# Performance work log

Measured on AMD Instinct MI355X. Metric: run time of the kernel, lower is better.

## Reference

```python
import jax, jax.numpy as jnp
import numpy as np

B, S, D = 2, 2048, 1024
H = 16
DK = D // H  # attn_dim // num_heads = 64
DV = D // H  # embed_dim // num_heads = 64
NEG = -1e9


def setup_inputs() -> dict:
    key = jax.random.key(0)
    ks = jax.random.split(key, 6)
    inputs = jax.random.normal(ks[0], (B, S, D), dtype=jnp.float32)
    # mask[b, i, j]: key position i may attend to query position j when i <= j (causal)
    mask = jnp.broadcast_to(jnp.triu(jnp.ones((S, S), dtype=bool))[None], (B, S, S))
    sd = 1.0 / np.sqrt(D)
    WQ = jax.random.normal(ks[1], (D, H, DK), dtype=jnp.float32) * sd
    WK = jax.random.normal(ks[2], (D, H, DK), dtype=jnp.float32) * sd
    WV = jax.random.normal(ks[3], (D, H, DV), dtype=jnp.float32) * sd
    WO = jax.random.normal(ks[4], (D, D), dtype=jnp.float32) * sd
    bO = jnp.zeros((D,), dtype=jnp.float32)
    return {"inputs": inputs, "mask": mask, "WQ": WQ, "WK": WK, "WV": WV, "WO": WO, "bO": bO}


def reference(inputs, mask, WQ, WK, WV, WO, bO):
    scale = 1.0 / jnp.sqrt(jnp.float32(DK))
    q = jnp.einsum('bid,dhk->bihk', inputs, WQ) * scale
    k = jnp.einsum('bid,dhk->bihk', inputs, WK)
    v = jnp.einsum('bid,dhv->bihv', inputs, WV)
    # scores: [b, i, j, h]; softmax over axis=1 (key axis i), as in the original
    scores = jnp.einsum('bihd,bjhd->bijh', q, k)
    scores = jnp.where(mask[..., None], scores, NEG)
    attn = jax.nn.softmax(scores, axis=1)
    x = jnp.einsum('bijh,bihv->bjhv', attn, v)  # output indexed by query j
    x = x.reshape(B, S, D)
    return x @ WO + bO
```

## Files before the change

### kernel.cpp

```cpp
#include <hip/hip_runtime.h>
#include <hip/hip_bf16.h>


typedef __bf16 bf16;
typedef __bf16 bf16x8 __attribute__((ext_vector_type(8)));
typedef __bf16 bf16x4 __attribute__((ext_vector_type(4)));
typedef float  f32x4  __attribute__((ext_vector_type(4)));

constexpr int Sq = 2048;
constexpr int Dm = 1024;
constexpr int Hh = 16;

__global__ __launch_bounds__(256) void cvt_bf16(
    const float* __restrict__ src, bf16* __restrict__ dst, int n) {
  const int i = (blockIdx.x * 256 + threadIdx.x) * 8;
  if (i >= n) return;
  float4 a = *reinterpret_cast<const float4*>(src + i);
  float4 b = *reinterpret_cast<const float4*>(src + i + 4);
  bf16x8 o;
  o[0] = (bf16)a.x; o[1] = (bf16)a.y; o[2] = (bf16)a.z; o[3] = (bf16)a.w;
  o[4] = (bf16)b.x; o[5] = (bf16)b.y; o[6] = (bf16)b.z; o[7] = (bf16)b.w;
  *reinterpret_cast<bf16x8*>(dst + i) = o;
}

__global__ __launch_bounds__(256) void tposeW4(
    const float* __restrict__ WQ, const float* __restrict__ WK,
    const float* __restrict__ WV, const float* __restrict__ WO,
    bf16* __restrict__ out) {
  __shared__ bf16 t[64][65];
  const int z = blockIdx.z;
  const float* in = (z == 0) ? WQ : (z == 1) ? WK : (z == 2) ? WV : WO;
  bf16* op = out + (size_t)z * 1024 * 1024;
  const int r0 = blockIdx.y * 64, c0 = blockIdx.x * 64;
  const int tid = threadIdx.x;
  const int rr = tid >> 3, cc = (tid & 7) * 8;
#pragma unroll
  for (int it = 0; it < 2; ++it) {
    int row = rr + it * 32;
    const float* ip = in + (size_t)(r0 + row) * 1024 + c0 + cc;
    float4 a = *reinterpret_cast<const float4*>(ip);
    float4 b = *reinterpret_cast<const float4*>(ip + 4);
    t[row][cc + 0] = (bf16)a.x; t[row][cc + 1] = (bf16)a.y;
    t[row][cc + 2] = (bf16)a.z; t[row][cc + 3] = (bf16)a.w;
    t[row][cc + 4] = (bf16)b.x; t[row][cc + 5] = (bf16)b.y;
    t[row][cc + 6] = (bf16)b.z; t[row][cc + 7] = (bf16)b.w;
  }
  __syncthreads();
#pragma unroll
  for (int it = 0; it < 2; ++it) {
    int crow = rr + it * 32;
    alignas(16) bf16 o[8];
#pragma unroll
    for (int e = 0; e < 8; ++e) o[e] = t[cc + e][crow];
    *reinterpret_cast<bf16x8*>(op + (size_t)(c0 + crow) * 1024 + r0 + cc) =
        *reinterpret_cast<bf16x8*>(o);
  }
}

template <int EPI>
__global__ __launch_bounds__(256) void gemm128(
    const bf16* __restrict__ A, const bf16* __restrict__ Bt,
    const int M, const int N, const int K,
    bf16* __restrict__ Katt, bf16* __restrict__ Qatt, bf16* __restrict__ VattT,
    const float* __restrict__ bOf, float* __restrict__ Cout) {
  __shared__ bf16 As[8192], Bs[8192];
  const int tid = threadIdx.x;
  const int lane = tid & 63;
  const int w = tid >> 6;
  const int wr = w >> 1, wc = w & 1;
  const int g = lane >> 4, c = lane & 15;
  const int m0 = blockIdx.y * 128, n0 = blockIdx.x * 128;

  f32x4 acc[4][4];
#pragma unroll
  for (int i = 0; i < 4; ++i)
#pragma unroll
    for (int j = 0; j < 4; ++j) acc[i][j] = f32x4{0.f, 0.f, 0.f, 0.f};

  const int trow = tid >> 3, tch = tid & 7;
  for (int k0 = 0; k0 < K; k0 += 64) {
#pragma unroll
    for (int p = 0; p < 4; ++p) {
      int row = trow + p * 32;
      *reinterpret_cast<bf16x8*>(&As[row * 64 + ((tch ^ (row & 7)) << 3)]) =
          *reinterpret_cast<const bf16x8*>(A + (size_t)(m0 + row) * K + k0 + tch * 8);
      *reinterpret_cast<bf16x8*>(&Bs[row * 64 + ((tch ^ (row & 7)) << 3)]) =
          *reinterpret_cast<const bf16x8*>(Bt + (size_t)(n0 + row) * K + k0 + tch * 8);
    }
    __syncthreads();
#pragma unroll
    for (int kk = 0; kk < 2; ++kk) {
      const int ch = kk * 4 + g;
      bf16x8 af[4], bfr[4];
#pragma unroll
      for (int mf = 0; mf < 4; ++mf) {
        int row = wr * 64 + mf * 16 + c;
        af[mf] = *reinterpret_cast<const bf16x8*>(&As[row * 64 + ((ch ^ (row & 7)) << 3)]);
      }
#pragma unroll
      for (int nf = 0; nf < 4; ++nf) {
        int row = wc * 64 + nf * 16 + c;
        bfr[nf] = *reinterpret_cast<const bf16x8*>(&Bs[row * 64 + ((ch ^ (row & 7)) << 3)]);
      }
#pragma unroll
      for (int mf = 0; mf < 4; ++mf)
#pragma unroll
        for (int nf = 0; nf < 4; ++nf)
          acc[mf][nf] = __builtin_amdgcn_mfma_f32_16x16x32_bf16(
              af[mf], bfr[nf], acc[mf][nf], 0, 0, 0);
    }
    __syncthreads();
  }

#pragma unroll
  for (int mf = 0; mf < 4; ++mf)
#pragma unroll
    for (int nf = 0; nf < 4; ++nf) {
      const int n = n0 + wc * 64 + nf * 16 + c;
      const int mb = m0 + wr * 64 + mf * 16 + g * 4;
      if (EPI == 0 && n >= 2048) {
        bf16x4 pk;
#pragma unroll
        for (int r = 0; r < 4; ++r) pk[r] = (bf16)acc[mf][nf][r];
        const int b = mb >> 11, sb = mb & (Sq - 1);
        const int h = (n >> 6) & 15, dk = n & 63;
        *reinterpret_cast<bf16x4*>(
            &VattT[((size_t)(b * Hh + h) * 64 + dk) * Sq + sb]) = pk;
      } else {
#pragma unroll
        for (int r = 0; r < 4; ++r) {
          const int m = mb + r;
          float v = acc[mf][nf][r];
          if (EPI == 0) {
            const int b = m >> 11, s = m & (Sq - 1);
            const int h = (n >> 6) & 15, dk = n & 63;
            const int bh = b * Hh + h;
            if (n < 1024)
              Katt[((size_t)bh * Sq + s) * 64 + dk] = (bf16)(v * 0.125f);
            else
              Qatt[((size_t)bh * Sq + s) * 64 + dk] = (bf16)v;
          } else {
            Cout[(size_t)m * N + n] = v + bOf[n];
          }
        }
      }
    }
}

__global__ __launch_bounds__(256, 4) void attn_v4(
    const bf16* __restrict__ Q, const bf16* __restrict__ K,
    const bf16* __restrict__ Vt, bf16* __restrict__ X) {
  __shared__ bf16 Kb[2][4096];
  __shared__ bf16 Vb[2][4096];
  __shared__ bf16 Pb[4096];
  const int tid = threadIdx.x, lane = tid & 63, w = tid >> 6;
  const int g = lane >> 4, c = lane & 15;
  const int bx = blockIdx.x;
  const int u = bx >> 5;
  const int bh = bx & 31;
  const int um = (u + 8 * (bh >> 3)) & 31;
  const int qblk = (um < 16) ? um : 47 - um;
  const int b = bh >> 4, h = bh & 15;
  const size_t base = (size_t)bh * Sq * 64;
  const bf16* Kg = K + base;
  const bf16* Vg = Vt + (size_t)bh * 64 * Sq;
  const int trow = tid >> 3, tch = tid & 7;
  bf16* Pw = Pb + w * 16 * 64;

  bf16x8 qf[2];
  {
    const bf16* Qg = Q + base + ((size_t)qblk * 64 + w * 16 + c) * 64;
    qf[0] = *reinterpret_cast<const bf16x8*>(Qg + g * 8);
    qf[1] = *reinterpret_cast<const bf16x8*>(Qg + 32 + g * 8);
  }

#pragma unroll
  for (int pp = 0; pp < 2; ++pp) {
    int row = trow + pp * 32;
    *reinterpret_cast<bf16x8*>(&Kb[0][row * 64 + ((tch ^ (row & 7)) << 3)]) =
        *reinterpret_cast<const bf16x8*>(Kg + (size_t)row * 64 + tch * 8);
    *reinterpret_cast<bf16x8*>(&Vb[0][row * 64 + ((tch ^ (row & 7)) << 3)]) =
        *reinterpret_cast<const bf16x8*>(Vg + (size_t)row * Sq + tch * 8);
  }
  __syncthreads();

  f32x4 acc[4];
  float lpart[4] = {0.f, 0.f, 0.f, 0.f};
#pragma unroll
  for (int vg = 0; vg < 4; ++vg) acc[vg] = f32x4{0.f, 0.f, 0.f, 0.f};

  const int ntiles = qblk + 1;
  for (int t = 0; t < ntiles; ++t) {
    const int cur = t & 1;
    const bf16* Kc = Kb[cur];
    const bf16* Vc = Vb[cur];
    const bool hasnext = (t + 1 < ntiles);

    bf16x8 kr0, kr1, vr0, vr1;
    if (hasnext) {
      const int i1 = (t + 1) * 64;
      kr0 = *reinterpret_cast<const bf16x8*>(Kg + (size_t)(i1 + trow) * 64 + tch * 8);
      kr1 = *reinterpret_cast<const bf16x8*>(Kg + (size_t)(i1 + trow + 32) * 64 + tch * 8);
      vr0 = *reinterpret_cast<const bf16x8*>(Vg + (size_t)trow * Sq + i1 + tch * 8);
      vr1 = *reinterpret_cast<const bf16x8*>(Vg + (size_t)(trow + 32) * Sq + i1 + tch * 8);
    }

    f32x4 sc[4];
#pragma unroll
    for (int kg = 0; kg < 4; ++kg) sc[kg] = f32x4{0.f, 0.f, 0.f, 0.f};
#pragma unroll
    for (int kk = 0; kk < 2; ++kk) {
      const int ch = kk * 4 + g;
#pragma unroll
      for (int kg = 0; kg < 4; ++kg) {
        int row = kg * 16 + c;
        bf16x8 kf = *reinterpret_cast<const bf16x8*>(
            &Kc[row * 64 + ((ch ^ (row & 7)) << 3)]);
        sc[kg] = __builtin_amdgcn_mfma_f32_16x16x32_bf16(qf[kk], kf, sc[kg], 0, 0, 0);
      }
    }

    const bool diag = (t == qblk);
#pragma unroll
    for (int kg = 0; kg < 4; ++kg)
#pragma unroll
      for (int r = 0; r < 4; ++r) {
        float p = __expf(sc[kg][r]);
        if (diag) {
          const int i = kg * 16 + c;
          const int j = w * 16 + g * 4 + r;
          p = (i <= j) ? p : 0.f;
        }
        lpart[r] += p;
        const int prow = g * 4 + r, pcol = kg * 16 + c;
        Pw[prow * 64 + (((pcol >> 3) ^ (prow & 7)) << 3) + (pcol & 7)] = (bf16)p;
      }

#pragma unroll
    for (int ks = 0; ks < 2; ++ks) {
      const int ch = ks * 4 + g;
      bf16x8 pf = *reinterpret_cast<const bf16x8*>(
          &Pw[c * 64 + ((ch ^ (c & 7)) << 3)]);
#pragma unroll
      for (int vg = 0; vg < 4; ++vg) {
        int dv = vg * 16 + c;
        bf16x8 vf = *reinterpret_cast<const bf16x8*>(
            &Vc[dv * 64 + ((ch ^ (dv & 7)) << 3)]);
        acc[vg] = __builtin_amdgcn_mfma_f32_16x16x32_bf16(pf, vf, acc[vg], 0, 0, 0);
      }
    }

    if (hasnext) {
      bf16* Kn = Kb[cur ^ 1];
      bf16* Vn = Vb[cur ^ 1];
      const int row0 = trow, row1 = trow + 32;
      *reinterpret_cast<bf16x8*>(&Kn[row0 * 64 + ((tch ^ (row0 & 7)) << 3)]) = kr0;
      *reinterpret_cast<bf16x8*>(&Kn[row1 * 64 + ((tch ^ (row1 & 7)) << 3)]) = kr1;
      *reinterpret_cast<bf16x8*>(&Vn[row0 * 64 + ((tch ^ (row0 & 7)) << 3)]) = vr0;
      *reinterpret_cast<bf16x8*>(&Vn[row1 * 64 + ((tch ^ (row1 & 7)) << 3)]) = vr1;
    }
    __syncthreads();
  }

  float linv[4];
#pragma unroll
  for (int r = 0; r < 4; ++r) {
    float l = lpart[r];
    l += __shfl_xor(l, 1);
    l += __shfl_xor(l, 2);
    l += __shfl_xor(l, 4);
    l += __shfl_xor(l, 8);
    linv[r] = 1.f / l;
  }
#pragma unroll
  for (int vg = 0; vg < 4; ++vg)
#pragma unroll
    for (int r = 0; r < 4; ++r) {
      const int j = qblk * 64 + w * 16 + g * 4 + r;
      const int dv = vg * 16 + c;
      X[((size_t)b * Sq + j) * Dm + h * 64 + dv] = (bf16)(acc[vg][r] * linv[r]);
    }
}

extern "C" void kernel_launch(void* const* d_in, const int* in_sizes, int n_in,
                              void* d_out, int out_size, void* d_ws, size_t ws_size,
                              hipStream_t stream) {
  const float* inputs = (const float*)d_in[0];
  const float* WQ = (const float*)d_in[2];
  const float* WK = (const float*)d_in[3];
  const float* WV = (const float*)d_in[4];
  const float* WO = (const float*)d_in[5];
  const float* bO = (const float*)d_in[6];
  float* out = (float*)d_out;

  bf16* Xin   = (bf16*)d_ws;
  bf16* Wt    = Xin + 4096 * 1024;
  bf16* Katt  = Wt + 4 * 1024 * 1024;
  bf16* Qatt  = Katt + (1 << 22);
  bf16* VattT = Qatt + (1 << 22);
  bf16* X     = Xin;

  cvt_bf16<<<2048, 256, 0, stream>>>(inputs, Xin, 4096 * 1024);

  tposeW4<<<dim3(16, 16, 4), 256, 0, stream>>>(WQ, WK, WV, WO, Wt);

  gemm128<0><<<dim3(24, 32), 256, 0, stream>>>(
      Xin, Wt, 4096, 3072, 1024, Katt, Qatt, VattT, nullptr, nullptr);

  attn_v4<<<dim3(1024), 256, 0, stream>>>(Qatt, Katt, VattT, X);

  gemm128<1><<<dim3(8, 32), 256, 0, stream>>>(
      X, Wt + 3 * 1024 * 1024, 4096, 1024, 1024,
      nullptr, nullptr, nullptr, bO, out);
}
```

Baseline: 115.1 us.

## Load GEMM tiles via direct global-to-LDS loads and fold log2e into K scale

The GEMM tile staging now uses global_load_lds, which writes global data straight into shared memory without passing through registers. Because of this, the XOR swizzle on the LDS layout is dropped and fragment reads use plain row-major offsets, which may bring back LDS bank conflicts. Separately, log2(e) is folded into the K scaling factor so that softmax can call exp2f instead of __expf, saving a multiply per element.

After: 137.1 us. 1.19x slower.

```diff
diff --git a/kernel.cpp b/kernel.cpp
--- a/kernel.cpp
+++ b/kernel.cpp
@@ -10,6 +10,14 @@
 constexpr int Sq = 2048;
 constexpr int Dm = 1024;
 constexpr int Hh = 16;
+
+#define KSCALE 0.18033688011112042f
+
+static __device__ __forceinline__ void gload_lds16(const bf16* g, bf16* l) {
+  __builtin_amdgcn_global_load_lds(
+      (const __attribute__((address_space(1))) unsigned int*)g,
+      (__attribute__((address_space(3))) unsigned int*)l, 16, 0, 0);
+}
 
 __global__ __launch_bounds__(256) void cvt_bf16(
     const float* __restrict__ src, bf16* __restrict__ dst, int n) {
@@ -70,6 +78,8 @@
   const int wr = w >> 1, wc = w & 1;
   const int g = lane >> 4, c = lane & 15;
   const int m0 = blockIdx.y * 128, n0 = blockIdx.x * 128;
+  const int sr = lane >> 3;
+  const int sc8 = (lane & 7) * 8;
 
   f32x4 acc[4][4];
 #pragma unroll
@@ -77,15 +87,12 @@
 #pragma unroll
     for (int j = 0; j < 4; ++j) acc[i][j] = f32x4{0.f, 0.f, 0.f, 0.f};
 
-  const int trow = tid >> 3, tch = tid & 7;
   for (int k0 = 0; k0 < K; k0 += 64) {
 #pragma unroll
     for (int p = 0; p < 4; ++p) {
-      int row = trow + p * 32;
-      *reinterpret_cast<bf16x8*>(&As[row * 64 + ((tch ^ (row & 7)) << 3)]) =
-          *reinterpret_cast<const bf16x8*>(A + (size_t)(m0 + row) * K + k0 + tch * 8);
-      *reinterpret_cast<bf16x8*>(&Bs[row * 64 + ((tch ^ (row & 7)) << 3)]) =
-          *reinterpret_cast<const bf16x8*>(Bt + (size_t)(n0 + row) * K + k0 + tch * 8);
+      const int rowb = p * 32 + w * 8;
+      gload_lds16(A + (size_t)(m0 + rowb + sr) * K + k0 + sc8, &As[rowb * 64]);
+      gload_lds16(Bt + (size_t)(n0 + rowb + sr) * K + k0 + sc8, &Bs[rowb * 64]);
     }
     __syncthreads();
 #pragma unroll
@@ -93,15 +100,13 @@
       const int ch = kk * 4 + g;
       bf16x8 af[4], bfr[4];
 #pragma unroll
-      for (int mf = 0; mf < 4; ++mf) {
-        int row = wr * 64 + mf * 16 + c;
-        af[mf] = *reinterpret_cast<const bf16x8*>(&As[row * 64 + ((ch ^ (row & 7)) << 3)]);
-      }
-#pragma unroll
-      for (int nf = 0; nf < 4; ++nf) {
-        int row = wc * 64 + nf * 16 + c;
-        bfr[nf] = *reinterpret_cast<const bf16x8*>(&Bs[row * 64 + ((ch ^ (row & 7)) << 3)]);
-      }
+      for (int mf = 0; mf < 4; ++mf)
+        af[mf] = *reinterpret_cast<const bf16x8*>(
+            &As[(wr * 64 + mf * 16 + c) * 64 + ch * 8]);
+#pragma unroll
+      for (int nf = 0; nf < 4; ++nf)
+        bfr[nf] = *reinterpret_cast<const bf16x8*>(
+            &Bs[(wc * 64 + nf * 16 + c) * 64 + ch * 8]);
 #pragma unroll
       for (int mf = 0; mf < 4; ++mf)
 #pragma unroll
@@ -136,7 +141,7 @@
             const int h = (n >> 6) & 15, dk = n & 63;
             const int bh = b * Hh + h;
             if (n < 1024)
-              Katt[((size_t)bh * Sq + s) * 64 + dk] = (bf16)(v * 0.125f);
+              Katt[((size_t)bh * Sq + s) * 64 + dk] = (bf16)(v * KSCALE);
             else
               Qatt[((size_t)bh * Sq + s) * 64 + dk] = (bf16)v;
           } else {
@@ -225,7 +230,7 @@
     for (int kg = 0; kg < 4; ++kg)
 #pragma unroll
       for (int r = 0; r < 4; ++r) {
-        float p = __expf(sc[kg][r]);
+        float p = exp2f(sc[kg][r]);
         if (diag) {
           const int i = kg * 16 + c;
           const int j = w * 16 + g * 4 + r;
```
